# Performance work log

Measured on AMD Instinct MI355X. Metric: run time of the kernel, lower is better.

Reference implementation:

```python
import jax, jax.numpy as jnp
import numpy as np

N_HEAD = 16
NEG_INF = -1e9


def setup_inputs() -> dict:
    key = jax.random.key(0)
    k1, k2, k3 = jax.random.split(key, 3)
    B, S, D = 4, 1024, 1024
    x = jax.random.normal(k1, (B, S, D), dtype=jnp.float32)
    w_attn = jax.random.normal(k2, (D, 3 * D), dtype=jnp.float32) * 0.02
    b_attn = jnp.zeros((3 * D,), dtype=jnp.float32)
    w_proj = jax.random.normal(k3, (D, D), dtype=jnp.float32) * 0.02
    b_proj = jnp.zeros((D,), dtype=jnp.float32)
    return {"x": x, "w_attn": w_attn, "b_attn": b_attn,
            "w_proj": w_proj, "b_proj": b_proj}


def reference(x, w_attn, b_attn, w_proj, b_proj):
    B, S, D = x.shape
    H = N_HEAD
    hd = D // H
    # fused QKV Conv1D: addmm over flattened tokens
    qkv = x @ w_attn + b_attn                      # [B,S,3D]
    q, k, v = jnp.split(qkv, 3, axis=-1)           # each [B,S,D]
    # split heads -> [B,H,S,hd]
    def heads(t):
        return t.reshape(B, S, H, hd).transpose(0, 2, 1, 3)
    q, k, v = heads(q), heads(k), heads(v)
    # scaled dot-product with causal mask
    scores = jnp.einsum('bhqd,bhkd->bhqk', q, k) / jnp.sqrt(jnp.float32(hd))
    causal = jnp.tril(jnp.ones((S, S), dtype=bool))[None, None]  # [1,1,S,S]
    scores = jnp.where(causal, scores, NEG_INF)
    attn = jax.nn.softmax(scores, axis=-1)
    out = jnp.einsum('bhqk,bhkd->bhqd', attn, v)   # [B,H,S,hd]
    out = out.transpose(0, 2, 1, 3).reshape(B, S, D)  # merge heads
    # output projection Conv1D
    return out @ w_proj + b_proj
```

## Files before the change

### kernel.cpp

```cpp
#include <hip/hip_runtime.h>
#include <hip/hip_bf16.h>

typedef __attribute__((ext_vector_type(8))) __bf16 bf16x8;
typedef __attribute__((ext_vector_type(4))) float f32x4;

__device__ __forceinline__ unsigned short f2bf(float f) {
  unsigned int u = __builtin_bit_cast(unsigned int, f);
  u += 0x7fffu + ((u >> 16) & 1u);
  return (unsigned short)(u >> 16);
}

__device__ __forceinline__ unsigned int cvtpk_bf16(float a, float b) {
  unsigned int r;
  asm("v_cvt_pk_bf16_f32 %0, %1, %2" : "=v"(r) : "v"(a), "v"(b));
  return r;
}

__device__ __forceinline__ void gll16(const void* g, void* l) {
  __builtin_amdgcn_global_load_lds(
      (const __attribute__((address_space(1))) void*)g,
      (__attribute__((address_space(3))) void*)l, 16, 0, 0);
}

__device__ __forceinline__ bf16x8 lds_frag(const unsigned short* base, int row, int kbyte) {
  int off = row * 128 + (kbyte ^ ((row & 7) << 4));
  return *(const bf16x8*)((const char*)base + off);
}

#define QUAD(AF, BV, MO)                                                       \
  asm volatile("s_waitcnt lgkmcnt(0)" ::: "memory");                           \
  __builtin_amdgcn_sched_barrier(0);                                           \
  __builtin_amdgcn_s_setprio(1);                                               \
  _Pragma("unroll") for (int j = 0; j < 4; ++j)                                \
      _Pragma("unroll") for (int ni = 0; ni < 4; ++ni)                         \
          acc[MO + j][ni] = __builtin_amdgcn_mfma_f32_16x16x32_bf16(           \
              AF[j], BV[ni], acc[MO + j][ni], 0, 0, 0);                        \
  __builtin_amdgcn_s_setprio(0);                                               \
  __builtin_amdgcn_sched_barrier(0);

__global__ __launch_bounds__(256) void cast_bf16(const float* __restrict__ in,
                                                 unsigned short* __restrict__ out, int n) {
  int i = (blockIdx.x * 256 + threadIdx.x) * 4;
  if (i < n) {
    float4 v = *(const float4*)(in + i);
    ushort4 o;
    o.x = f2bf(v.x); o.y = f2bf(v.y); o.z = f2bf(v.z); o.w = f2bf(v.w);
    *(ushort4*)(out + i) = o;
  }
}

__global__ __launch_bounds__(256) void transpose_cast(const float* __restrict__ in,
                                                      unsigned short* __restrict__ out,
                                                      int K, int N) {
  __shared__ float tile[32][33];
  int nb = N >> 5;
  int bx = blockIdx.x % nb, by = blockIdx.x / nb;
  int n0 = bx << 5, k0 = by << 5;
  int c = threadIdx.x & 31, r0 = threadIdx.x >> 5;
#pragma unroll
  for (int i = 0; i < 4; ++i) {
    int r = r0 + i * 8;
    tile[r][c] = in[(size_t)(k0 + r) * N + n0 + c];
  }
  __syncthreads();
#pragma unroll
  for (int i = 0; i < 4; ++i) {
    int r = r0 + i * 8;
    out[(size_t)(n0 + r) * K + k0 + c] = f2bf(tile[c][r]);
  }
}

__global__ __launch_bounds__(512, 2) void gemm_qkv256(
    const unsigned short* __restrict__ A, const unsigned short* __restrict__ Bt,
    const float* __restrict__ bias,
    unsigned short* __restrict__ Qg, unsigned short* __restrict__ Kg,
    unsigned short* __restrict__ Vtg, int K) {
  __shared__ __align__(16) unsigned short SMEM[65536];
  unsigned short* const A0 = SMEM;
  unsigned short* const B0 = SMEM + 16384;
  unsigned short* const A1 = SMEM + 32768;
  unsigned short* const B1 = SMEM + 49152;
  const int t = threadIdx.x;
  const int l = t & 63, lr = l & 15, hi = l >> 4;
  const int w = t >> 6;
  const int wr = w >> 2, wc = w & 3;
  const int bid = (int)(blockIdx.x % 8) * 24 + (int)(blockIdx.x / 8);
  const int bm = bid / 12, bn = bid % 12;
  const int m0 = bm << 8, n0 = bn << 8;
  const int wbase = (t & ~63) * 8;

  f32x4 acc[8][4] = {};

  auto stage_half = [&](int kt, int h, unsigned short* Ad, unsigned short* Bd) {
    const unsigned short* src;
    unsigned short* dst;
    if (h < 2) { src = A  + (size_t)(m0 + h * 128) * K + kt * 64;       dst = Ad + h * 8192; }
    else       { src = Bt + (size_t)(n0 + (h - 2) * 128) * K + kt * 64; dst = Bd + (h - 2) * 8192; }
#pragma unroll
    for (int i = 0; i < 2; ++i) {
      int ci = i * 512 + t;
      int row = ci >> 3, cpos = ci & 7;
      int c = cpos ^ (row & 7);
      gll16(src + (size_t)row * K + c * 8, dst + i * 4096 + wbase);
    }
  };

  auto lda = [&](bf16x8* af, const unsigned short* Ac, int mo, int kb) {
#pragma unroll
    for (int j = 0; j < 4; ++j)
      af[j] = lds_frag(Ac, wr * 128 + (mo + j) * 16 + lr, kb + hi * 16);
  };
  auto ldb = [&](bf16x8* bv, const unsigned short* Bc, int kb) {
#pragma unroll
    for (int j = 0; j < 4; ++j)
      bv[j] = lds_frag(Bc, wc * 64 + j * 16 + lr, kb + hi * 16);
  };

  const int nt = K >> 6;
  stage_half(0, 0, A0, B0); stage_half(0, 1, A0, B0);
  stage_half(0, 2, A0, B0); stage_half(0, 3, A0, B0);

  for (int T = 0; T < nt; ++T) {
    const unsigned short* Ac = (T & 1) ? A1 : A0;
    const unsigned short* Bc = (T & 1) ? B1 : B0;
    unsigned short* An = (T & 1) ? A0 : A1;
    unsigned short* Bn = (T & 1) ? B0 : B1;
    const bool pf = (T + 1 < nt);

    if (pf) {
      stage_half(T + 1, 0, An, Bn);
      asm volatile("s_waitcnt vmcnt(2)" ::: "memory");
    } else {
      asm volatile("s_waitcnt vmcnt(0)" ::: "memory");
    }
    __builtin_amdgcn_s_barrier();

    bf16x8 af[4], bv[4];
    ldb(bv, Bc, 0);
    lda(af, Ac, 0, 0);
    if (pf) stage_half(T + 1, 1, An, Bn);
    __builtin_amdgcn_s_barrier();
    QUAD(af, bv, 0);
    __builtin_amdgcn_s_barrier();
    lda(af, Ac, 4, 0);
    if (pf) stage_half(T + 1, 2, An, Bn);
    __builtin_amdgcn_s_barrier();
    QUAD(af, bv, 4);
    __builtin_amdgcn_s_barrier();
    ldb(bv, Bc, 64);
    lda(af, Ac, 0, 64);
    if (pf) stage_half(T + 1, 3, An, Bn);
    __builtin_amdgcn_s_barrier();
    QUAD(af, bv, 0);
    __builtin_amdgcn_s_barrier();
    lda(af, Ac, 4, 64);
    __builtin_amdgcn_s_barrier();
    QUAD(af, bv, 4);
    __builtin_amdgcn_s_barrier();
  }

  if (n0 < 2048) {
    const float QSCALE = 0.125f * 1.4426950408889634f;
#pragma unroll
    for (int mi = 0; mi < 8; ++mi)
#pragma unroll
      for (int ni = 0; ni < 4; ++ni)
#pragma unroll
        for (int r = 0; r < 4; ++r) {
          int m = m0 + wr * 128 + mi * 16 + 4 * hi + r;
          int n = n0 + wc * 64 + ni * 16 + lr;
          float v = acc[mi][ni][r] + bias[n];
          int b = m >> 10, s = m & 1023;
          int d = n & 1023;
          int h = d >> 6, di = d & 63;
          int bh = (b << 4) + h;
          if (n < 1024) Qg[((size_t)(bh << 10) + s) * 64 + di] = f2bf(v * QSCALE);
          else          Kg[((size_t)(bh << 10) + s) * 64 + di] = f2bf(v);
        }
  } else {
    __syncthreads();
#pragma unroll
    for (int mi = 0; mi < 8; ++mi)
#pragma unroll
      for (int ni = 0; ni < 4; ++ni) {
        int nl = wc * 64 + ni * 16 + lr;
        int ml = wr * 128 + mi * 16 + 4 * hi;
        ushort4 pk;
        pk.x = f2bf(acc[mi][ni][0] + bias[n0 + nl]);
        pk.y = f2bf(acc[mi][ni][1] + bias[n0 + nl]);
        pk.z = f2bf(acc[mi][ni][2] + bias[n0 + nl]);
        pk.w = f2bf(acc[mi][ni][3] + bias[n0 + nl]);
        *(ushort4*)&SMEM[nl * 256 + (ml ^ ((nl & 7) << 3))] = pk;
      }
    __syncthreads();
    const int b = m0 >> 10;
    const int sbase = m0 & 1023;
#pragma unroll
    for (int it = 0; it < 16; ++it) {
      int nl = it * 16 + (t >> 5);
      int s0 = (t & 31) * 8;
      bf16x8 v8 = *(const bf16x8*)&SMEM[nl * 256 + (s0 ^ ((nl & 7) << 3))];
      int d = n0 - 2048 + nl;
      size_t row = ((size_t)((b << 4) + (d >> 6)) << 6) + (d & 63);
      *(bf16x8*)&Vtg[row * 1024 + sbase + s0] = v8;
    }
  }
}

__global__ __launch_bounds__(256, 2) void gemm_proj128(
    const unsigned short* __restrict__ A, const unsigned short* __restrict__ Bt,
    const float* __restrict__ bias, float* __restrict__ outf,
    int M, int N, int K) {
  __shared__ unsigned short A0[128 * 64], B0[128 * 64];
  __shared__ unsigned short A1[128 * 64], B1[128 * 64];
  const int t = threadIdx.x;
  const int w = t >> 6, l = t & 63, lr = l & 15, hi = l >> 4;
  const int wr = w >> 1, wc = w & 1;
  const int nbn = N >> 7;
  const int nwg = (M >> 7) * nbn;
  int bid = (int)blockIdx.x;
  if ((nwg & 7) == 0) bid = (bid % 8) * (nwg / 8) + bid / 8;
  const int bm = bid / nbn, bn = bid % nbn;
  const int m0 = bm << 7, n0 = bn << 7;
  const int wbase = (t & ~63) * 8;

  f32x4 acc[4][4] = {};

  auto stage_half = [&](int kt, int h, unsigned short* Ad, unsigned short* Bd) {
    const unsigned short* src;
    unsigned short* dst;
    if (h < 2) { src = A  + (size_t)(m0 + h * 64) * K + kt * 64;       dst = Ad + h * 4096; }
    else       { src = Bt + (size_t)(n0 + (h - 2) * 64) * K + kt * 64; dst = Bd + (h - 2) * 4096; }
#pragma unroll
    for (int i = 0; i < 2; ++i) {
      int ci = i * 256 + t;
      int row = ci >> 3, cpos = ci & 7;
      int c = cpos ^ (row & 7);
      gll16(src + (size_t)row * K + c * 8, dst + i * 2048 + wbase);
    }
  };

  auto lda = [&](bf16x8* af, const unsigned short* Ac, int kb) {
#pragma unroll
    for (int j = 0; j < 4; ++j)
      af[j] = lds_frag(Ac, wr * 64 + j * 16 + lr, kb + hi * 16);
  };
  auto ldb = [&](bf16x8* bv, const unsigned short* Bc, int kb) {
#pragma unroll
    for (int j = 0; j < 4; ++j)
      bv[j] = lds_frag(Bc, wc * 64 + j * 16 + lr, kb + hi * 16);
  };

  const int nt = K >> 6;
  stage_half(0, 0, A0, B0); stage_half(0, 1, A0, B0);
  stage_half(0, 2, A0, B0); stage_half(0, 3, A0, B0);

  for (int T = 0; T < nt; ++T) {
    const unsigned short* Ac = (T & 1) ? A1 : A0;
    const unsigned short* Bc = (T & 1) ? B1 : B0;
    unsigned short* An = (T & 1) ? A0 : A1;
    unsigned short* Bn = (T & 1) ? B0 : B1;
    const bool pf = (T + 1 < nt);

    if (pf) {
      stage_half(T + 1, 0, An, Bn);
      asm volatile("s_waitcnt vmcnt(2)" ::: "memory");
    } else {
      asm volatile("s_waitcnt vmcnt(0)" ::: "memory");
    }
    __builtin_amdgcn_s_barrier();

    bf16x8 af[4], bv[4];
    ldb(bv, Bc, 0);
    lda(af, Ac, 0);
    if (pf) { stage_half(T + 1, 2, An, Bn); stage_half(T + 1, 1, An, Bn); }
    __builtin_amdgcn_s_barrier();
    QUAD(af, bv, 0);
    __builtin_amdgcn_s_barrier();
    ldb(bv, Bc, 64);
    lda(af, Ac, 64);
    if (pf) stage_half(T + 1, 3, An, Bn);
    __builtin_amdgcn_s_barrier();
    QUAD(af, bv, 0);
    __builtin_amdgcn_s_barrier();
  }

#pragma unroll
  for (int mi = 0; mi < 4; ++mi)
#pragma unroll
    for (int ni = 0; ni < 4; ++ni)
#pragma unroll
      for (int r = 0; r < 4; ++r) {
        int m = m0 + wr * 64 + mi * 16 + 4 * hi + r;
        int n = n0 + wc * 64 + ni * 16 + lr;
        outf[(size_t)m * N + n] = acc[mi][ni][r] + bias[n];
      }
}

__global__ __launch_bounds__(256) void attn_kernel(
    const unsigned short* __restrict__ Qg, const unsigned short* __restrict__ Kg,
    const unsigned short* __restrict__ Vtg, unsigned short* __restrict__ Og) {
  __shared__ unsigned short Klds[2][64 * 64];
  __shared__ unsigned short Vlds[2][64 * 64];
  __shared__ __align__(16) unsigned short Plds[4][16][72];
  const int bh = blockIdx.x & 63;
  const int qt = blockIdx.x >> 6;
  const int t = threadIdx.x;
  const int w = t >> 6, l = t & 63, lr = l & 15, hi = l >> 4;
  const unsigned short* Qbh = Qg + (size_t)bh * 65536;
  const unsigned short* Kbh = Kg + (size_t)bh * 65536;
  const unsigned short* Vbh = Vtg + (size_t)bh * 65536;
  const int q0 = qt * 64 + w * 16;
  const int wbase = (t & ~63) * 8;

  bf16x8 qf[2];
#pragma unroll
  for (int ks = 0; ks < 2; ++ks)
    qf[ks] = *(const bf16x8*)(Qbh + (size_t)(q0 + lr) * 64 + ks * 32 + hi * 8);

  f32x4 ocT[4] = {};
  float mrun = -1e30f, lrun = 0.f;
  const int thr = w * 16 + lr - 4 * hi;

  auto stage = [&](int kt, int b) {
#pragma unroll
    for (int i = 0; i < 2; ++i) {
      int ci = i * 256 + t;
      int row = ci >> 3, cpos = ci & 7;
      int c = cpos ^ (row & 7);
      gll16(Kbh + (size_t)(kt * 64 + row) * 64 + c * 8, &Klds[b][i * 2048 + wbase]);
      gll16(Vbh + (size_t)row * 1024 + kt * 64 + c * 8, &Vlds[b][i * 2048 + wbase]);
    }
  };

  stage(0, 0);
  __syncthreads();

  for (int kt = 0; kt <= qt; ++kt) {
    const int cur = kt & 1;
    if (kt < qt) stage(kt + 1, cur ^ 1);

    f32x4 sc[4] = {};
    __builtin_amdgcn_s_setprio(1);
#pragma unroll
    for (int c = 0; c < 4; ++c)
#pragma unroll
      for (int ks = 0; ks < 2; ++ks) {
        bf16x8 kf = lds_frag(&Klds[cur][0], c * 16 + lr, ks * 64 + hi * 16);
        sc[c] = __builtin_amdgcn_mfma_f32_16x16x32_bf16(kf, qf[ks], sc[c], 0, 0, 0);
      }
    __builtin_amdgcn_s_setprio(0);
    if (kt == qt) {
#pragma unroll
      for (int c = 0; c < 4; ++c)
#pragma unroll
        for (int r = 0; r < 4; ++r)
          if (c * 16 + r > thr) sc[c][r] = -1e30f;
    }

    float mx = sc[0][0];
#pragma unroll
    for (int c = 0; c < 4; ++c)
#pragma unroll
      for (int r = 0; r < 4; ++r) mx = fmaxf(mx, sc[c][r]);
    mx = fmaxf(mx, __shfl_xor(mx, 16));
    mx = fmaxf(mx, __shfl_xor(mx, 32));
    float mn = fmaxf(mrun, mx);
    float al = exp2f(mrun - mn);
    mrun = mn;
    float p[4][4], s = 0.f;
#pragma unroll
    for (int c = 0; c < 4; ++c)
#pragma unroll
      for (int r = 0; r < 4; ++r) {
        p[c][r] = exp2f(sc[c][r] - mn);
        s += p[c][r];
      }
    s += __shfl_xor(s, 16);
    s += __shfl_xor(s, 32);
    lrun = lrun * al + s;
#pragma unroll
    for (int c = 0; c < 4; ++c)
#pragma unroll
      for (int r = 0; r < 4; ++r) ocT[c][r] *= al;

#pragma unroll
    for (int c = 0; c < 4; ++c) {
      uint2 pk;
      pk.x = cvtpk_bf16(p[c][0], p[c][1]);
      pk.y = cvtpk_bf16(p[c][2], p[c][3]);
      *(uint2*)&Plds[w][lr][c * 16 + 4 * hi] = pk;
    }
    asm volatile("s_waitcnt lgkmcnt(0)" ::: "memory");
    __builtin_amdgcn_sched_barrier(0);

    bf16x8 pb[2];
#pragma unroll
    for (int ks = 0; ks < 2; ++ks)
      pb[ks] = *(const bf16x8*)(&Plds[w][lr][ks * 32 + hi * 8]);
    __builtin_amdgcn_s_setprio(1);
#pragma unroll
    for (int c = 0; c < 4; ++c)
#pragma unroll
      for (int ks = 0; ks < 2; ++ks) {
        bf16x8 vf = lds_frag(&Vlds[cur][0], c * 16 + lr, ks * 64 + hi * 16);
        ocT[c] = __builtin_amdgcn_mfma_f32_16x16x32_bf16(vf, pb[ks], ocT[c], 0, 0, 0);
      }
    __builtin_amdgcn_s_setprio(0);
    __syncthreads();
  }

  const int b = bh >> 4, h = bh & 15;
  const float inv = 1.0f / lrun;
  const size_t rowbase = ((size_t)(b * 1024 + q0 + lr)) * 1024 + h * 64;
#pragma unroll
  for (int c = 0; c < 4; ++c) {
    uint2 o2;
    o2.x = cvtpk_bf16(ocT[c][0] * inv, ocT[c][1] * inv);
    o2.y = cvtpk_bf16(ocT[c][2] * inv, ocT[c][3] * inv);
    *(uint2*)&Og[rowbase + c * 16 + 4 * hi] = o2;
  }
}

extern "C" void kernel_launch(void* const* d_in, const int* in_sizes, int n_in,
                              void* d_out, int out_size, void* d_ws, size_t ws_size,
                              hipStream_t stream) {
  const float* x      = (const float*)d_in[0];
  const float* w_attn = (const float*)d_in[1];
  const float* b_attn = (const float*)d_in[2];
  const float* w_proj = (const float*)d_in[3];
  const float* b_proj = (const float*)d_in[4];
  float* out = (float*)d_out;

  unsigned short* ws  = (unsigned short*)d_ws;
  unsigned short* xb  = ws;
  unsigned short* waT = xb + 4096 * 1024;
  unsigned short* wpT = waT + 3072 * 1024;
  unsigned short* Qg  = wpT + 1024 * 1024;
  unsigned short* Kg  = Qg + 4194304;
  unsigned short* Vtg = Kg + 4194304;
  unsigned short* Og  = xb;

  cast_bf16<<<4096, 256, 0, stream>>>(x, xb, 4194304);
  transpose_cast<<<(3072 / 32) * (1024 / 32), 256, 0, stream>>>(w_attn, waT, 1024, 3072);
  transpose_cast<<<(1024 / 32) * (1024 / 32), 256, 0, stream>>>(w_proj, wpT, 1024, 1024);

  gemm_qkv256<<<16 * 12, 512, 0, stream>>>(xb, waT, b_attn, Qg, Kg, Vtg, 1024);
  attn_kernel<<<1024, 256, 0, stream>>>(Qg, Kg, Vtg, Og);
  gemm_proj128<<<32 * 8, 256, 0, stream>>>(Og, wpT, b_proj, (float*)out, 4096, 1024, 1024);
}
```

Measured before the change: 104.1 us.

## Fuse prep kernels, split K/V staging in attention, skip redundant softmax rescale

Merges the bf16 cast and the two weight transpose-casts into a single prep launch, which removes two kernel launches. In the attention kernel, K stays double-buffered while V uses a single buffer staged after the PV MFMA, synchronised with explicit vmcnt waits and barriers; this cuts LDS use and the full barrier. Online-softmax rescaling of the accumulator is also skipped when no row maximum grew, avoiding exp and multiply work. The extra barriers and the single V buffer can expose V load latency.

```diff
diff --git a/kernel.cpp b/kernel.cpp
--- a/kernel.cpp
+++ b/kernel.cpp
@@ -38,25 +38,31 @@
   __builtin_amdgcn_s_setprio(0);                                               \
   __builtin_amdgcn_sched_barrier(0);
 
-__global__ __launch_bounds__(256) void cast_bf16(const float* __restrict__ in,
-                                                 unsigned short* __restrict__ out, int n) {
-  int i = (blockIdx.x * 256 + threadIdx.x) * 4;
-  if (i < n) {
-    float4 v = *(const float4*)(in + i);
+__global__ __launch_bounds__(256) void prep(
+    const float* __restrict__ x, unsigned short* __restrict__ xb,
+    const float* __restrict__ wa, unsigned short* __restrict__ waT,
+    const float* __restrict__ wp, unsigned short* __restrict__ wpT) {
+  __shared__ float tile[32][33];
+  const int b = blockIdx.x;
+  const int t = threadIdx.x;
+  if (b < 4096) {
+    int i = (b * 256 + t) * 4;
+    float4 v = *(const float4*)(x + i);
     ushort4 o;
     o.x = f2bf(v.x); o.y = f2bf(v.y); o.z = f2bf(v.z); o.w = f2bf(v.w);
-    *(ushort4*)(out + i) = o;
-  }
-}
-
-__global__ __launch_bounds__(256) void transpose_cast(const float* __restrict__ in,
-                                                      unsigned short* __restrict__ out,
-                                                      int K, int N) {
-  __shared__ float tile[32][33];
+    *(ushort4*)(xb + i) = o;
+    return;
+  }
+  const float* in;
+  unsigned short* out;
+  int bid, N;
+  if (b < 7168) { in = wa; out = waT; bid = b - 4096; N = 3072; }
+  else          { in = wp; out = wpT; bid = b - 7168; N = 1024; }
+  const int K = 1024;
   int nb = N >> 5;
-  int bx = blockIdx.x % nb, by = blockIdx.x / nb;
+  int bx = bid % nb, by = bid / nb;
   int n0 = bx << 5, k0 = by << 5;
-  int c = threadIdx.x & 31, r0 = threadIdx.x >> 5;
+  int c = t & 31, r0 = t >> 5;
 #pragma unroll
   for (int i = 0; i < 4; ++i) {
     int r = r0 + i * 8;
@@ -300,8 +306,8 @@
 __global__ __launch_bounds__(256) void attn_kernel(
     const unsigned short* __restrict__ Qg, const unsigned short* __restrict__ Kg,
     const unsigned short* __restrict__ Vtg, unsigned short* __restrict__ Og) {
-  __shared__ unsigned short Klds[2][64 * 64];
-  __shared__ unsigned short Vlds[2][64 * 64];
+  __shared__ unsigned short K0[64 * 64], K1[64 * 64];
+  __shared__ unsigned short Vb[64 * 64];
   __shared__ __align__(16) unsigned short Plds[4][16][72];
   const int bh = blockIdx.x & 63;
   const int qt = blockIdx.x >> 6;
@@ -322,23 +328,37 @@
   float mrun = -1e30f, lrun = 0.f;
   const int thr = w * 16 + lr - 4 * hi;
 
-  auto stage = [&](int kt, int b) {
+  auto stageK = [&](int kt, unsigned short* Kd) {
 #pragma unroll
     for (int i = 0; i < 2; ++i) {
       int ci = i * 256 + t;
       int row = ci >> 3, cpos = ci & 7;
       int c = cpos ^ (row & 7);
-      gll16(Kbh + (size_t)(kt * 64 + row) * 64 + c * 8, &Klds[b][i * 2048 + wbase]);
-      gll16(Vbh + (size_t)row * 1024 + kt * 64 + c * 8, &Vlds[b][i * 2048 + wbase]);
-    }
-  };
-
-  stage(0, 0);
-  __syncthreads();
+      gll16(Kbh + (size_t)(kt * 64 + row) * 64 + c * 8, Kd + i * 2048 + wbase);
+    }
+  };
+  auto stageV = [&](int kt) {
+#pragma unroll
+    for (int i = 0; i < 2; ++i) {
+      int ci = i * 256 + t;
+      int row = ci >> 3, cpos = ci & 7;
+      int c = cpos ^ (row & 7);
+      gll16(Vbh + (size_t)row * 1024 + kt * 64 + c * 8, Vb + i * 2048 + wbase);
+    }
+  };
+
+  stageK(0, K0);
+  stageV(0);
 
   for (int kt = 0; kt <= qt; ++kt) {
-    const int cur = kt & 1;
-    if (kt < qt) stage(kt + 1, cur ^ 1);
+    unsigned short* Kc = (kt & 1) ? K1 : K0;
+    unsigned short* Kn = (kt & 1) ? K0 : K1;
+    const bool pf = (kt < qt);
+
+    asm volatile("s_waitcnt vmcnt(2)" ::: "memory");
+    __builtin_amdgcn_s_barrier();
+
+    if (pf) stageK(kt + 1, Kn);
 
     f32x4 sc[4] = {};
     __builtin_amdgcn_s_setprio(1);
@@ -346,7 +366,7 @@
     for (int c = 0; c < 4; ++c)
 #pragma unroll
       for (int ks = 0; ks < 2; ++ks) {
-        bf16x8 kf = lds_frag(&Klds[cur][0], c * 16 + lr, ks * 64 + hi * 16);
+        bf16x8 kf = lds_frag(Kc, c * 16 + lr, ks * 64 + hi * 16);
         sc[c] = __builtin_amdgcn_mfma_f32_16x16x32_bf16(kf, qf[ks], sc[c], 0, 0, 0);
       }
     __builtin_amdgcn_s_setprio(0);
@@ -365,24 +385,27 @@
       for (int r = 0; r < 4; ++r) mx = fmaxf(mx, sc[c][r]);
     mx = fmaxf(mx, __shfl_xor(mx, 16));
     mx = fmaxf(mx, __shfl_xor(mx, 32));
-    float mn = fmaxf(mrun, mx);
-    float al = exp2f(mrun - mn);
-    mrun = mn;
+    if (!__all(mx <= mrun)) {
+      float mn = fmaxf(mrun, mx);
+      float al = exp2f(mrun - mn);
+      mrun = mn;
+      lrun *= al;
+#pragma unroll
+      for (int c = 0; c < 4; ++c)
+#pragma unroll
+        for (int r = 0; r < 4; ++r) ocT[c][r] *= al;
+    }
     float p[4][4], s = 0.f;
 #pragma unroll
     for (int c = 0; c < 4; ++c)
 #pragma unroll
       for (int r = 0; r < 4; ++r) {
-        p[c][r] = exp2f(sc[c][r] - mn);
+        p[c][r] = exp2f(sc[c][r] - mrun);
         s += p[c][r];
       }
     s += __shfl_xor(s, 16);
     s += __shfl_xor(s, 32);
-    lrun = lrun * al + s;
-#pragma unroll
-    for (int c = 0; c < 4; ++c)
-#pragma unroll
-      for (int r = 0; r < 4; ++r) ocT[c][r] *= al;
+    lrun += s;
 
 #pragma unroll
     for (int c = 0; c < 4; ++c) {
@@ -398,16 +421,22 @@
 #pragma unroll
     for (int ks = 0; ks < 2; ++ks)
       pb[ks] = *(const bf16x8*)(&Plds[w][lr][ks * 32 + hi * 8]);
+
+    if (pf) asm volatile("s_waitcnt vmcnt(2)" ::: "memory");
+    else    asm volatile("s_waitcnt vmcnt(0)" ::: "memory");
+    __builtin_amdgcn_s_barrier();
+
     __builtin_amdgcn_s_setprio(1);
 #pragma unroll
     for (int c = 0; c < 4; ++c)
 #pragma unroll
       for (int ks = 0; ks < 2; ++ks) {
-        bf16x8 vf = lds_frag(&Vlds[cur][0], c * 16 + lr, ks * 64 + hi * 16);
+        bf16x8 vf = lds_frag(Vb, c * 16 + lr, ks * 64 + hi * 16);
         ocT[c] = __builtin_amdgcn_mfma_f32_16x16x32_bf16(vf, pb[ks], ocT[c], 0, 0, 0);
       }
     __builtin_amdgcn_s_setprio(0);
-    __syncthreads();
+    __builtin_amdgcn_s_barrier();
+    if (pf) stageV(kt + 1);
   }
 
   const int b = bh >> 4, h = bh & 15;
@@ -441,10 +470,7 @@
   unsigned short* Vtg = Kg + 4194304;
   unsigned short* Og  = xb;
 
-  cast_bf16<<<4096, 256, 0, stream>>>(x, xb, 4194304);
-  transpose_cast<<<(3072 / 32) * (1024 / 32), 256, 0, stream>>>(w_attn, waT, 1024, 3072);
-  transpose_cast<<<(1024 / 32) * (1024 / 32), 256, 0, stream>>>(w_proj, wpT, 1024, 1024);
-
+  prep<<<8192, 256, 0, stream>>>(x, xb, w_attn, waT, w_proj, wpT);
   gemm_qkv256<<<16 * 12, 512, 0, stream>>>(xb, waT, b_attn, Qg, Kg, Vtg, 1024);
   attn_kernel<<<1024, 256, 0, stream>>>(Qg, Kg, Vtg, Og);
   gemm_proj128<<<32 * 8, 256, 0, stream>>>(Og, wpT, b_proj, (float*)out, 4096, 1024, 1024);
```

Result: faster. 100.3 us (-3.6%).
